# Kernel optimization log

Hardware: AMD Instinct MI355X
Metric: run time of the kernel (lower is better)

Reference implementation:

```python
import jax, jax.numpy as jnp
import numpy as np

HEADS = 4
KS = 7          # neighborhood kernel size
EPS = 1e-5
C = 64
N, H, W = 8, 64, 64


def _gather_idx(L, k):
    # NATTEN-style neighborhood: window centered at pixel, shifted to stay in bounds.
    start = jnp.clip(jnp.arange(L) - k // 2, 0, L - k)            # [L]
    idx = start[:, None] + jnp.arange(k)                           # [L, k] absolute neighbor idx
    # relative-position-bias index: (query - neighbor) + (k-1) in [0, 2k-2]
    rel = (jnp.arange(L) - start)[:, None] + (k - 1) - jnp.arange(k)[None, :]  # [L, k]
    return idx, rel


def na2d(x, qkv_w, qkv_b, rpb, proj_w, proj_b):
    # x: [N, H, W, C] -> neighborhood attention with rel-pos bias
    n, h, w, c = x.shape
    hd = c // HEADS
    scale = hd ** -0.5
    qkv = (x @ qkv_w.T + qkv_b).reshape(n, h, w, 3, HEADS, hd)
    q = qkv[..., 0, :, :] * scale                                  # [n,h,w,heads,hd]
    k = qkv[..., 1, :, :]
    v = qkv[..., 2, :, :]
    idx_h, rel_h = _gather_idx(h, KS)
    idx_w, rel_w = _gather_idx(w, KS)
    # gather neighborhoods: [n, h, k, w, k, heads, hd]
    kg = k[:, idx_h][:, :, :, idx_w]
    vg = v[:, idx_h][:, :, :, idx_w]
    attn = jnp.einsum('nijhd,niajbhd->nijhab', q, kg)              # [n,h,w,heads,k,k]
    bias = rpb[:, rel_h, :]                                        # [heads, h, k, 2k-1]
    bias = jnp.take(bias, rel_w, axis=-1)                          # [heads, h, k, w, k]
    bias = jnp.transpose(bias, (1, 3, 0, 2, 4))                    # [h, w, heads, k, k]
    attn = attn + bias
    a = jax.nn.softmax(attn.reshape(n, h, w, HEADS, KS * KS), axis=-1).reshape(attn.shape)
    out = jnp.einsum('nijhab,niajbhd->nijhd', a, vg).reshape(n, h, w, c)
    return out @ proj_w.T + proj_b


def setup_inputs() -> dict:
    key = jax.random.key(0)
    ks = jax.random.split(key, 12)
    s = 0.02
    return {
        'x': jax.random.normal(ks[0], (N, C, H, W), jnp.float32),
        'gn_w': jnp.ones((C,), jnp.float32),
        'gn_b': jnp.zeros((C,), jnp.float32),
        'qkv_w': jax.random.normal(ks[1], (3 * C, C), jnp.float32) * s,
        'qkv_b': jnp.zeros((3 * C,), jnp.float32),
        'rpb': jax.random.normal(ks[2], (HEADS, 2 * KS - 1, 2 * KS - 1), jnp.float32) * s,
        'proj_w': jax.random.normal(ks[3], (C, C), jnp.float32) * s,
        'proj_b': jnp.zeros((C,), jnp.float32),
        'ln_w': jnp.ones((C,), jnp.float32),
        'ln_b': jnp.zeros((C,), jnp.float32),
        'fc1_w': jax.random.normal(ks[4], (4 * C, C), jnp.float32) * s,
        'fc1_b': jnp.zeros((4 * C,), jnp.float32),
        'fc2_w': jax.random.normal(ks[5], (C, 4 * C), jnp.float32) * s,
        'fc2_b': jnp.zeros((C,), jnp.float32),
    }


def reference(x, gn_w, gn_b, qkv_w, qkv_b, rpb, proj_w, proj_b,
              ln_w, ln_b, fc1_w, fc1_b, fc2_w, fc2_b):
    n, c, h, w = x.shape
    x1 = jnp.transpose(x, (0, 2, 3, 1))                            # residual, NHWC
    # GroupNorm(1, C): normalize over (C,H,W) per sample, per-channel affine
    mu = jnp.mean(x, axis=(1, 2, 3), keepdims=True)
    var = jnp.var(x, axis=(1, 2, 3), keepdims=True)
    xg = (x - mu) * jax.lax.rsqrt(var + EPS)
    xg = xg * gn_w[None, :, None, None] + gn_b[None, :, None, None]
    xg = jnp.transpose(xg, (0, 2, 3, 1))                           # NHWC
    y = na2d(xg, qkv_w, qkv_b, rpb, proj_w, proj_b) + x1           # [n,h,w,c]
    y = y.reshape(n, h * w, c)
    # LayerNorm over channels + MLP (GELU), residual
    mu2 = jnp.mean(y, axis=-1, keepdims=True)
    var2 = jnp.var(y, axis=-1, keepdims=True)
    yn = (y - mu2) * jax.lax.rsqrt(var2 + EPS) * ln_w + ln_b
    hdn = jax.nn.gelu(yn @ fc1_w.T + fc1_b, approximate=False)
    y = y + (hdn @ fc2_w.T + fc2_b)
    return jnp.transpose(y.reshape(n, h, w, c), (0, 3, 1, 2))      # back to NCHW
```

## Files before the change

kernel.cpp:

```cpp
#include <hip/hip_runtime.h>
#include <math.h>

#define NSAMP 8
#define CH 64
#define HH 64
#define WW 64
#define SPATIAL 4096
#define PER_SAMPLE 262144
#define NTOK 32768
#define NHEADS 4
#define HD 16
#define KS 7
#define EPS 1e-5f
#define QSCALE 0.25f

typedef __attribute__((ext_vector_type(8))) short short8;
typedef __attribute__((ext_vector_type(4))) float f32x4;
typedef _Float16 hf2 __attribute__((ext_vector_type(2)));

__device__ __forceinline__ unsigned short f2bf(float f) {
    unsigned u = __float_as_uint(f);
    u = u + 0x7fffu + ((u >> 16) & 1u);
    return (unsigned short)(u >> 16);
}
__device__ __forceinline__ unsigned pack2(float a, float b) {
    return (unsigned)f2bf(a) | ((unsigned)f2bf(b) << 16);
}
__device__ __forceinline__ unsigned short f2h(float f) {
    _Float16 h = (_Float16)f;
    return __builtin_bit_cast(unsigned short, h);
}
__device__ __forceinline__ unsigned pack2h(float a, float b) {
    return (unsigned)f2h(a) | ((unsigned)f2h(b) << 16);
}
__device__ __forceinline__ hf2 u2h(unsigned u) { return __builtin_bit_cast(hf2, u); }

__device__ __forceinline__ float dot8_h(uint4 k, uint4 q) {
    hf2 a0 = u2h(k.x), a1 = u2h(k.y), a2 = u2h(k.z), a3 = u2h(k.w);
    hf2 b0 = u2h(q.x), b1 = u2h(q.y), b2 = u2h(q.z), b3 = u2h(q.w);
    float s;
    s = (float)a0.x * (float)b0.x;
    s = fmaf((float)a0.y, (float)b0.y, s);
    s = fmaf((float)a1.x, (float)b1.x, s);
    s = fmaf((float)a1.y, (float)b1.y, s);
    s = fmaf((float)a2.x, (float)b2.x, s);
    s = fmaf((float)a2.y, (float)b2.y, s);
    s = fmaf((float)a3.x, (float)b3.x, s);
    s = fmaf((float)a3.y, (float)b3.y, s);
    return s;
}
__device__ __forceinline__ void pv8_h(uint4 v, float p, float* acc) {
    hf2 a0 = u2h(v.x), a1 = u2h(v.y), a2 = u2h(v.z), a3 = u2h(v.w);
    acc[0] = fmaf(p, (float)a0.x, acc[0]);
    acc[1] = fmaf(p, (float)a0.y, acc[1]);
    acc[2] = fmaf(p, (float)a1.x, acc[2]);
    acc[3] = fmaf(p, (float)a1.y, acc[3]);
    acc[4] = fmaf(p, (float)a2.x, acc[4]);
    acc[5] = fmaf(p, (float)a2.y, acc[5]);
    acc[6] = fmaf(p, (float)a3.x, acc[6]);
    acc[7] = fmaf(p, (float)a3.y, acc[7]);
}

__global__ __launch_bounds__(256) void k_statsprep(const float* __restrict__ x,
                                                   float* __restrict__ stats,
                                                   const float* __restrict__ qkv_w,
                                                   const float* __restrict__ fc1_w,
                                                   const float* __restrict__ fc2_w,
                                                   const float* __restrict__ proj_w,
                                                   unsigned short* __restrict__ wb) {
    int blk = blockIdx.x;
    if (blk >= 256) {
        int i = (blk - 256) * 256 + threadIdx.x;
        if (i < 12288)      wb[i] = f2bf(qkv_w[i]);
        else if (i < 28672) wb[i] = f2bf(fc1_w[i - 12288]);
        else if (i < 45056) wb[i] = f2bf(fc2_w[i - 28672]);
        else                wb[i] = f2bf(proj_w[i - 45056]);
        return;
    }
    int n = blk >> 5, chunk = blk & 31;
    const float4* p4 = (const float4*)(x + n * PER_SAMPLE + chunk * 8192);
    int t = threadIdx.x;
    float s1 = 0.f, s2 = 0.f;
#pragma unroll
    for (int i = 0; i < 8; i++) {
        float4 v = p4[t + i * 256];
        s1 += v.x + v.y + v.z + v.w;
        s2 += v.x * v.x + v.y * v.y + v.z * v.z + v.w * v.w;
    }
#pragma unroll
    for (int off = 1; off < 64; off <<= 1) {
        s1 += __shfl_xor(s1, off);
        s2 += __shfl_xor(s2, off);
    }
    __shared__ float r1[4], r2[4];
    int lane = t & 63, wv = t >> 6;
    if (lane == 0) { r1[wv] = s1; r2[wv] = s2; }
    __syncthreads();
    if (t == 0) {
        stats[(n * 32 + chunk) * 2 + 0] = r1[0] + r1[1] + r1[2] + r1[3];
        stats[(n * 32 + chunk) * 2 + 1] = r2[0] + r2[1] + r2[2] + r2[3];
    }
}

__global__ __launch_bounds__(256) void k_qkv(const float* __restrict__ x,
                                             const float* __restrict__ stats,
                                             const float* __restrict__ gn_w,
                                             const float* __restrict__ gn_b,
                                             const unsigned short* __restrict__ qkv_wb,
                                             const float* __restrict__ qkv_b,
                                             uint4* __restrict__ qb8,
                                             uint4* __restrict__ kvb8) {
    __shared__ __attribute__((aligned(16))) short xA[4 * 2 * 64 * 8];
    __shared__ float obuf[4][16 * 65];
    int s0 = blockIdx.x * 64;
    int smp = s0 >> 12, sp = s0 & 4095;
    int t = threadIdx.x, tok = t & 63, g = t >> 6;

    float ps1 = 0.f, ps2 = 0.f;
    {
        const float2* pp = (const float2*)stats + smp * 32;
#pragma unroll
        for (int i = 0; i < 32; i++) {
            float2 p = pp[i];
            ps1 += p.x;
            ps2 += p.y;
        }
    }
    float mu = ps1 * (1.f / (float)PER_SAMPLE);
    float var = ps2 * (1.f / (float)PER_SAMPLE) - mu * mu;
    float rstd = rsqrtf(var + EPS);

    {
        const float* xp = x + smp * PER_SAMPLE + sp + tok;
        float v[16];
#pragma unroll
        for (int i = 0; i < 16; i++) {
            int c = g * 16 + i;
            v[i] = (xp[(size_t)c * SPATIAL] - mu) * rstd * gn_w[c] + gn_b[c];
        }
#pragma unroll
        for (int e = 0; e < 2; e++) {
            int cb = 2 * g + e;
            int kf = cb >> 2, qq = cb & 3;
            uint4 p;
            p.x = pack2(v[e * 8 + 0], v[e * 8 + 1]);
            p.y = pack2(v[e * 8 + 2], v[e * 8 + 3]);
            p.z = pack2(v[e * 8 + 4], v[e * 8 + 5]);
            p.w = pack2(v[e * 8 + 6], v[e * 8 + 7]);
            int chunk = ((tok >> 4) * 2 + kf) * 64 + (tok & 15) + (qq << 4);
            *(uint4*)&xA[chunk * 8] = p;
        }
    }
    __syncthreads();

    int w = __builtin_amdgcn_readfirstlane(g);
    int lane = t & 63, nh = lane & 15, qd = lane >> 4;

    short8 af[8];
#pragma unroll
    for (int mt = 0; mt < 4; mt++)
#pragma unroll
        for (int kf = 0; kf < 2; kf++)
            af[mt * 2 + kf] = *(const short8*)&xA[((mt * 2 + kf) * 64 + lane) * 8];

    for (int nt = 0; nt < 3; nt++) {
        int n0 = w * 48 + nt * 16;
        const unsigned short* wp = qkv_wb + (size_t)(n0 + nh) * 64 + qd * 8;
        short8 b0 = *(const short8*)(wp);
        short8 b1 = *(const short8*)(wp + 32);
        float bias = qkv_b[n0 + nh];
        bool isq = (n0 < 64);
        f32x4 acc[4];
#pragma unroll
        for (int mt = 0; mt < 4; mt++) {
            f32x4 d = {0.f, 0.f, 0.f, 0.f};
            d = __builtin_amdgcn_mfma_f32_16x16x32_bf16(af[mt * 2 + 0], b0, d, 0, 0, 0);
            d = __builtin_amdgcn_mfma_f32_16x16x32_bf16(af[mt * 2 + 1], b1, d, 0, 0, 0);
            acc[mt] = d;
        }
#pragma unroll
        for (int mt = 0; mt < 4; mt++)
#pragma unroll
            for (int r = 0; r < 4; r++) {
                float vv = acc[mt][r] + bias;
                if (isq) vv *= QSCALE;
                obuf[w][nh * 65 + mt * 16 + qd * 4 + r] = vv;
            }
        __builtin_amdgcn_wave_barrier();
#pragma unroll
        for (int u = 0; u < 2; u++) {
            uint4 p;
            p.x = pack2h(obuf[w][(u * 8 + 0) * 65 + lane], obuf[w][(u * 8 + 1) * 65 + lane]);
            p.y = pack2h(obuf[w][(u * 8 + 2) * 65 + lane], obuf[w][(u * 8 + 3) * 65 + lane]);
            p.z = pack2h(obuf[w][(u * 8 + 4) * 65 + lane], obuf[w][(u * 8 + 5) * 65 + lane]);
            p.w = pack2h(obuf[w][(u * 8 + 6) * 65 + lane], obuf[w][(u * 8 + 7) * 65 + lane]);
            if (n0 < 64)
                qb8[(size_t)((n0 >> 3) + u) * NTOK + s0 + lane] = p;
            else if (n0 < 128)
                kvb8[(size_t)(((n0 - 64) >> 3) + u) * NTOK + s0 + lane] = p;
            else
                kvb8[(size_t)(8 + ((n0 - 128) >> 3) + u) * NTOK + s0 + lane] = p;
        }
        __builtin_amdgcn_wave_barrier();
    }
}

__global__ __launch_bounds__(256, 4) void k_fused(const uint4* __restrict__ qb8,
                                               const uint4* __restrict__ kvb8,
                                               const float* __restrict__ rpb,
                                               const unsigned short* __restrict__ proj_wb,
                                               const float* __restrict__ proj_b,
                                               const float* __restrict__ x,
                                               const float* __restrict__ ln_w,
                                               const float* __restrict__ ln_b,
                                               const unsigned short* __restrict__ fc1_wb,
                                               const float* __restrict__ fc1_b,
                                               const unsigned short* __restrict__ fc2_wb,
                                               const float* __restrict__ fc2_b,
                                               float* __restrict__ out) {
    __shared__ __attribute__((aligned(16))) short fragA[2 * 2 * 64 * 8];
    __shared__ __attribute__((aligned(16))) short lhA[2 * 8 * 64 * 8];
    __shared__ float obuf[4][16 * 33];
    __shared__ float red1[256], red2[256];
    int xcd = blockIdx.x & 7, idx = blockIdx.x >> 3;
    int half = idx & 1;
    int h = xcd * 8 + ((idx >> 1) & 7);
    int n = idx >> 4;
    int t = threadIdx.x, lane = t & 63;
    int g = __builtin_amdgcn_readfirstlane(t >> 6);
    int w2 = lane & 31;
    int dh = lane >> 5;
    int w = half * 32 + w2;
    int rowbase = n * 4096 + h * 64;
    int cb = 2 * g + dh;

    uint4 qa = qb8[(size_t)cb * NTOK + rowbase + w];
    int sh = min(max(h - 3, 0), HH - KS);
    int sw = min(max(w - 3, 0), WW - KS);

    float sum = 0.f;
    float acc[8];
#pragma unroll
    for (int i = 0; i < 8; i++) acc[i] = 0.f;

#pragma unroll
    for (int a = 0; a < 7; a++) {
        int nb = n * 4096 + (sh + a) * 64 + sw;
        const float* rp = rpb + (g * 13 + (h - sh + 6 - a)) * 13 + (w - sw + 6);
        const uint4* kp = kvb8 + (size_t)cb * NTOK + nb;
        const uint4* vp = kvb8 + (size_t)(8 + cb) * NTOK + nb;
#pragma unroll
        for (int bb = 0; bb < 7; bb++) {
            uint4 kv = kp[bb];
            uint4 vv = vp[bb];
            float dhalf = dot8_h(kv, qa);
            float d = dhalf + __shfl_xor(dhalf, 32);
            d += rp[-bb];
            float e = __expf(d);
            sum += e;
            pv8_h(vv, e, acc);
        }
    }
    float rs = 1.f / sum;

    const float* xr = x + n * PER_SAMPLE + h * 64 + w;
    float xres[8];
#pragma unroll
    for (int i = 0; i < 8; i++)
        xres[i] = xr[(size_t)(cb * 8 + i) * SPATIAL];

    {
        int kf = cb >> 2, qsel = cb & 3;
        uint4 p;
        p.x = pack2(acc[0] * rs, acc[1] * rs);
        p.y = pack2(acc[2] * rs, acc[3] * rs);
        p.z = pack2(acc[4] * rs, acc[5] * rs);
        p.w = pack2(acc[6] * rs, acc[7] * rs);
        *(uint4*)&fragA[(((w2 >> 4) * 2 + kf) * 64 + (w2 & 15) + (qsel << 4)) * 8] = p;
    }
    __syncthreads();

    int nh = lane & 15, qd = lane >> 4;
    float yreg[8];
    {
        short8 af[4];
#pragma unroll
        for (int mt = 0; mt < 2; mt++)
#pragma unroll
            for (int kf = 0; kf < 2; kf++)
                af[mt * 2 + kf] = *(const short8*)&fragA[((mt * 2 + kf) * 64 + lane) * 8];

        int n0 = g * 16;
        const unsigned short* wp = proj_wb + (size_t)(n0 + nh) * 64 + qd * 8;
        short8 b0 = *(const short8*)(wp);
        short8 b1 = *(const short8*)(wp + 32);
        float bias = proj_b[n0 + nh];
#pragma unroll
        for (int mt = 0; mt < 2; mt++) {
            f32x4 d = {0.f, 0.f, 0.f, 0.f};
            d = __builtin_amdgcn_mfma_f32_16x16x32_bf16(af[mt * 2 + 0], b0, d, 0, 0, 0);
            d = __builtin_amdgcn_mfma_f32_16x16x32_bf16(af[mt * 2 + 1], b1, d, 0, 0, 0);
#pragma unroll
            for (int r = 0; r < 4; r++)
                obuf[g][nh * 33 + mt * 16 + qd * 4 + r] = d[r] + bias;
        }
        __builtin_amdgcn_wave_barrier();
#pragma unroll
        for (int i = 0; i < 8; i++)
            yreg[i] = obuf[g][(dh * 8 + i) * 33 + w2] + xres[i];
    }

    {
        float s1 = 0.f, s2 = 0.f;
#pragma unroll
        for (int i = 0; i < 8; i++) { s1 += yreg[i]; s2 += yreg[i] * yreg[i]; }
        red1[t] = s1;
        red2[t] = s2;
        __syncthreads();
        float m1 = 0.f, m2 = 0.f;
#pragma unroll
        for (int u = 0; u < 8; u++) { m1 += red1[u * 32 + w2]; m2 += red2[u * 32 + w2]; }
        float mu = m1 * (1.f / 64.f);
        float rstd = rsqrtf(m2 * (1.f / 64.f) - mu * mu + EPS);
        float v[8];
#pragma unroll
        for (int i = 0; i < 8; i++) {
            int c = cb * 8 + i;
            v[i] = (yreg[i] - mu) * rstd * ln_w[c] + ln_b[c];
        }
        int kf = cb >> 2, qsel = cb & 3;
        uint4 p;
        p.x = pack2(v[0], v[1]);
        p.y = pack2(v[2], v[3]);
        p.z = pack2(v[4], v[5]);
        p.w = pack2(v[6], v[7]);
        *(uint4*)&fragA[(((w2 >> 4) * 2 + kf) * 64 + (w2 & 15) + (qsel << 4)) * 8] = p;
    }
    __syncthreads();

    {
        short8 yf[4];
#pragma unroll
        for (int mt = 0; mt < 2; mt++)
#pragma unroll
            for (int kf = 0; kf < 2; kf++)
                yf[mt * 2 + kf] = *(const short8*)&fragA[((mt * 2 + kf) * 64 + lane) * 8];

#pragma unroll
        for (int nt = 0; nt < 4; nt++) {
            int n0f = g * 64 + nt * 16;
            const unsigned short* wp = fc1_wb + (size_t)(n0f + nh) * 64 + qd * 8;
            short8 b0 = *(const short8*)(wp);
            short8 b1 = *(const short8*)(wp + 32);
            float bias = fc1_b[n0f + nh];
            int j = n0f + nh;
            int kfA = j >> 5, q2 = (j >> 3) & 3, jb = j & 7;
#pragma unroll
            for (int mt = 0; mt < 2; mt++) {
                f32x4 d = {0.f, 0.f, 0.f, 0.f};
                d = __builtin_amdgcn_mfma_f32_16x16x32_bf16(yf[mt * 2 + 0], b0, d, 0, 0, 0);
                d = __builtin_amdgcn_mfma_f32_16x16x32_bf16(yf[mt * 2 + 1], b1, d, 0, 0, 0);
#pragma unroll
                for (int r = 0; r < 4; r++) {
                    float hv = d[r] + bias;
                    float t2 = -1.5957691216f * fmaf(0.044715f * hv * hv, hv, hv);
                    hv = hv / (1.f + __expf(t2));
                    lhA[((mt * 8 + kfA) * 64 + (qd * 4 + r) + (q2 << 4)) * 8 + jb] = (short)f2bf(hv);
                }
            }
        }
    }
    __syncthreads();

    f32x4 acc2[2];
    acc2[0] = (f32x4){0.f, 0.f, 0.f, 0.f};
    acc2[1] = (f32x4){0.f, 0.f, 0.f, 0.f};
#pragma unroll
    for (int kfA = 0; kfA < 8; kfA++) {
        const unsigned short* wp = fc2_wb + (size_t)(g * 16 + nh) * 256 + kfA * 32 + qd * 8;
        short8 bb = *(const short8*)(wp);
#pragma unroll
        for (int mt = 0; mt < 2; mt++) {
            short8 a = *(const short8*)&lhA[((mt * 8 + kfA) * 64 + lane) * 8];
            acc2[mt] = __builtin_amdgcn_mfma_f32_16x16x32_bf16(a, bb, acc2[mt], 0, 0, 0);
        }
    }
#pragma unroll
    for (int mt = 0; mt < 2; mt++)
#pragma unroll
        for (int r = 0; r < 4; r++)
            obuf[g][nh * 33 + mt * 16 + qd * 4 + r] = acc2[mt][r];
    __builtin_amdgcn_wave_barrier();
    float* op = out + (size_t)n * PER_SAMPLE + h * 64 + w;
#pragma unroll
    for (int i = 0; i < 8; i++) {
        int c = cb * 8 + i;
        op[(size_t)c * SPATIAL] = obuf[g][(dh * 8 + i) * 33 + w2] + fc2_b[c] + yreg[i];
    }
}

extern "C" void kernel_launch(void* const* d_in, const int* in_sizes, int n_in,
                              void* d_out, int out_size, void* d_ws, size_t ws_size,
                              hipStream_t stream) {
    const float* x      = (const float*)d_in[0];
    const float* gn_w   = (const float*)d_in[1];
    const float* gn_b   = (const float*)d_in[2];
    const float* qkv_w  = (const float*)d_in[3];
    const float* qkv_b  = (const float*)d_in[4];
    const float* rpb    = (const float*)d_in[5];
    const float* proj_w = (const float*)d_in[6];
    const float* proj_b = (const float*)d_in[7];
    const float* ln_w   = (const float*)d_in[8];
    const float* ln_b   = (const float*)d_in[9];
    const float* fc1_w  = (const float*)d_in[10];
    const float* fc1_b  = (const float*)d_in[11];
    const float* fc2_w  = (const float*)d_in[12];
    const float* fc2_b  = (const float*)d_in[13];
    float* out = (float*)d_out;

    float* ws    = (float*)d_ws;
    float* stats = ws;
    uint4* qb8   = (uint4*)(ws + 512);
    uint4* kvb8  = qb8 + (size_t)8 * NTOK;
    unsigned short* wb = (unsigned short*)(kvb8 + (size_t)16 * NTOK);
    unsigned short* qkv_wb  = wb;
    unsigned short* fc1_wb  = wb + 12288;
    unsigned short* fc2_wb  = wb + 28672;
    unsigned short* proj_wb = wb + 45056;

    k_statsprep<<<448, 256, 0, stream>>>(x, stats, qkv_w, fc1_w, fc2_w, proj_w, wb);
    k_qkv      <<<512, 256, 0, stream>>>(x, stats, gn_w, gn_b, qkv_wb, qkv_b, qb8, kvb8);
    k_fused    <<<1024, 256, 0, stream>>>(qb8, kvb8, rpb, proj_wb, proj_b, x,
                                          ln_w, ln_b, fc1_wb, fc1_b, fc2_wb, fc2_b, out);
}
```

Baseline: 123.1 us.

## Split fused attention+MLP kernel across 512 threads with 4-dim per-lane work

Doubles the fused kernel's block size to 512 threads. Each lane now handles 4 head dims instead of 8, with an extra cross-lane shuffle to complete the dot product. The MFMA stages are split so each wave pair processes one 16-token tile instead of two. The aim is more parallelism and latency hiding in the neighborhood attention loop. The cost is extra shuffles, narrower 8-byte loads, and more LDS for the reduction buffers.

```diff
diff --git a/kernel.cpp b/kernel.cpp
--- a/kernel.cpp
+++ b/kernel.cpp
@@ -35,30 +35,22 @@
 }
 __device__ __forceinline__ hf2 u2h(unsigned u) { return __builtin_bit_cast(hf2, u); }
 
-__device__ __forceinline__ float dot8_h(uint4 k, uint4 q) {
-    hf2 a0 = u2h(k.x), a1 = u2h(k.y), a2 = u2h(k.z), a3 = u2h(k.w);
-    hf2 b0 = u2h(q.x), b1 = u2h(q.y), b2 = u2h(q.z), b3 = u2h(q.w);
+__device__ __forceinline__ float dot4_h(uint2 k, uint2 q) {
+    hf2 a0 = u2h(k.x), a1 = u2h(k.y);
+    hf2 b0 = u2h(q.x), b1 = u2h(q.y);
     float s;
     s = (float)a0.x * (float)b0.x;
     s = fmaf((float)a0.y, (float)b0.y, s);
     s = fmaf((float)a1.x, (float)b1.x, s);
     s = fmaf((float)a1.y, (float)b1.y, s);
-    s = fmaf((float)a2.x, (float)b2.x, s);
-    s = fmaf((float)a2.y, (float)b2.y, s);
-    s = fmaf((float)a3.x, (float)b3.x, s);
-    s = fmaf((float)a3.y, (float)b3.y, s);
     return s;
 }
-__device__ __forceinline__ void pv8_h(uint4 v, float p, float* acc) {
-    hf2 a0 = u2h(v.x), a1 = u2h(v.y), a2 = u2h(v.z), a3 = u2h(v.w);
+__device__ __forceinline__ void pv4_h(uint2 v, float p, float* acc) {
+    hf2 a0 = u2h(v.x), a1 = u2h(v.y);
     acc[0] = fmaf(p, (float)a0.x, acc[0]);
     acc[1] = fmaf(p, (float)a0.y, acc[1]);
     acc[2] = fmaf(p, (float)a1.x, acc[2]);
     acc[3] = fmaf(p, (float)a1.y, acc[3]);
-    acc[4] = fmaf(p, (float)a2.x, acc[4]);
-    acc[5] = fmaf(p, (float)a2.y, acc[5]);
-    acc[6] = fmaf(p, (float)a3.x, acc[6]);
-    acc[7] = fmaf(p, (float)a3.y, acc[7]);
 }
 
 __global__ __launch_bounds__(256) void k_statsprep(const float* __restrict__ x,
@@ -205,7 +197,7 @@
     }
 }
 
-__global__ __launch_bounds__(256, 4) void k_fused(const uint4* __restrict__ qb8,
+__global__ __launch_bounds__(512, 8) void k_fused(const uint4* __restrict__ qb8,
                                                const uint4* __restrict__ kvb8,
                                                const float* __restrict__ rpb,
                                                const unsigned short* __restrict__ proj_wb,
@@ -220,132 +212,126 @@
                                                float* __restrict__ out) {
     __shared__ __attribute__((aligned(16))) short fragA[2 * 2 * 64 * 8];
     __shared__ __attribute__((aligned(16))) short lhA[2 * 8 * 64 * 8];
-    __shared__ float obuf[4][16 * 33];
-    __shared__ float red1[256], red2[256];
+    __shared__ float obuf[8][16 * 17];
+    __shared__ float red1[512], red2[512];
     int xcd = blockIdx.x & 7, idx = blockIdx.x >> 3;
     int half = idx & 1;
     int h = xcd * 8 + ((idx >> 1) & 7);
     int n = idx >> 4;
     int t = threadIdx.x, lane = t & 63;
-    int g = __builtin_amdgcn_readfirstlane(t >> 6);
-    int w2 = lane & 31;
-    int dh = lane >> 5;
+    int g2 = __builtin_amdgcn_readfirstlane(t >> 6);
+    int g = g2 >> 1;
+    int th = g2 & 1;
+    int w2t = lane & 15;
+    int q = lane >> 4;
+    int w2 = th * 16 + w2t;
     int w = half * 32 + w2;
     int rowbase = n * 4096 + h * 64;
-    int cb = 2 * g + dh;
-
-    uint4 qa = qb8[(size_t)cb * NTOK + rowbase + w];
+    int cb = 2 * g + (q >> 1);
+    int qsub = q & 1;
+
+    uint2 qa = ((const uint2*)qb8)[((size_t)cb * NTOK + rowbase + w) * 2 + qsub];
     int sh = min(max(h - 3, 0), HH - KS);
     int sw = min(max(w - 3, 0), WW - KS);
+    const uint2* kp2 = (const uint2*)(kvb8 + (size_t)cb * NTOK);
+    const uint2* vp2 = (const uint2*)(kvb8 + (size_t)(8 + cb) * NTOK);
 
     float sum = 0.f;
-    float acc[8];
-#pragma unroll
-    for (int i = 0; i < 8; i++) acc[i] = 0.f;
+    float acc[4];
+#pragma unroll
+    for (int i = 0; i < 4; i++) acc[i] = 0.f;
 
 #pragma unroll
     for (int a = 0; a < 7; a++) {
         int nb = n * 4096 + (sh + a) * 64 + sw;
         const float* rp = rpb + (g * 13 + (h - sh + 6 - a)) * 13 + (w - sw + 6);
-        const uint4* kp = kvb8 + (size_t)cb * NTOK + nb;
-        const uint4* vp = kvb8 + (size_t)(8 + cb) * NTOK + nb;
 #pragma unroll
         for (int bb = 0; bb < 7; bb++) {
-            uint4 kv = kp[bb];
-            uint4 vv = vp[bb];
-            float dhalf = dot8_h(kv, qa);
-            float d = dhalf + __shfl_xor(dhalf, 32);
+            uint2 kv = kp2[(size_t)(nb + bb) * 2 + qsub];
+            uint2 vv = vp2[(size_t)(nb + bb) * 2 + qsub];
+            float dq = dot4_h(kv, qa);
+            float d = dq + __shfl_xor(dq, 16);
+            d += __shfl_xor(d, 32);
             d += rp[-bb];
             float e = __expf(d);
             sum += e;
-            pv8_h(vv, e, acc);
+            pv4_h(vv, e, acc);
         }
     }
     float rs = 1.f / sum;
 
     const float* xr = x + n * PER_SAMPLE + h * 64 + w;
-    float xres[8];
-#pragma unroll
-    for (int i = 0; i < 8; i++)
-        xres[i] = xr[(size_t)(cb * 8 + i) * SPATIAL];
-
-    {
-        int kf = cb >> 2, qsel = cb & 3;
-        uint4 p;
-        p.x = pack2(acc[0] * rs, acc[1] * rs);
-        p.y = pack2(acc[2] * rs, acc[3] * rs);
-        p.z = pack2(acc[4] * rs, acc[5] * rs);
-        p.w = pack2(acc[6] * rs, acc[7] * rs);
-        *(uint4*)&fragA[(((w2 >> 4) * 2 + kf) * 64 + (w2 & 15) + (qsel << 4)) * 8] = p;
+    float xres[4];
+#pragma unroll
+    for (int i = 0; i < 4; i++)
+        xres[i] = xr[(size_t)(g * 16 + q * 4 + i) * SPATIAL];
+
+    int kf = cb >> 2, qsel = cb & 3;
+    int chunk = ((w2 >> 4) * 2 + kf) * 64 + (w2 & 15) + (qsel << 4);
+    {
+        uint2 p2;
+        p2.x = pack2(acc[0] * rs, acc[1] * rs);
+        p2.y = pack2(acc[2] * rs, acc[3] * rs);
+        *(uint2*)&fragA[chunk * 8 + qsub * 4] = p2;
     }
     __syncthreads();
 
     int nh = lane & 15, qd = lane >> 4;
-    float yreg[8];
-    {
-        short8 af[4];
-#pragma unroll
-        for (int mt = 0; mt < 2; mt++)
-#pragma unroll
-            for (int kf = 0; kf < 2; kf++)
-                af[mt * 2 + kf] = *(const short8*)&fragA[((mt * 2 + kf) * 64 + lane) * 8];
-
+    float yreg[4];
+    {
+        short8 af0 = *(const short8*)&fragA[((th * 2 + 0) * 64 + lane) * 8];
+        short8 af1 = *(const short8*)&fragA[((th * 2 + 1) * 64 + lane) * 8];
         int n0 = g * 16;
         const unsigned short* wp = proj_wb + (size_t)(n0 + nh) * 64 + qd * 8;
         short8 b0 = *(const short8*)(wp);
         short8 b1 = *(const short8*)(wp + 32);
         float bias = proj_b[n0 + nh];
-#pragma unroll
-        for (int mt = 0; mt < 2; mt++) {
-            f32x4 d = {0.f, 0.f, 0.f, 0.f};
-            d = __builtin_amdgcn_mfma_f32_16x16x32_bf16(af[mt * 2 + 0], b0, d, 0, 0, 0);
-            d = __builtin_amdgcn_mfma_f32_16x16x32_bf16(af[mt * 2 + 1], b1, d, 0, 0, 0);
-#pragma unroll
-            for (int r = 0; r < 4; r++)
-                obuf[g][nh * 33 + mt * 16 + qd * 4 + r] = d[r] + bias;
-        }
+        f32x4 d = {0.f, 0.f, 0.f, 0.f};
+        d = __builtin_amdgcn_mfma_f32_16x16x32_bf16(af0, b0, d, 0, 0, 0);
+        d = __builtin_amdgcn_mfma_f32_16x16x32_bf16(af1, b1, d, 0, 0, 0);
+#pragma unroll
+        for (int r = 0; r < 4; r++)
+            obuf[g2][nh * 17 + qd * 4 + r] = d[r] + bias;
         __builtin_amdgcn_wave_barrier();
 #pragma unroll
-        for (int i = 0; i < 8; i++)
-            yreg[i] = obuf[g][(dh * 8 + i) * 33 + w2] + xres[i];
+        for (int i = 0; i < 4; i++)
+            yreg[i] = obuf[g2][(q * 4 + i) * 17 + w2t] + xres[i];
     }
 
     {
         float s1 = 0.f, s2 = 0.f;
 #pragma unroll
-        for (int i = 0; i < 8; i++) { s1 += yreg[i]; s2 += yreg[i] * yreg[i]; }
+        for (int i = 0; i < 4; i++) { s1 += yreg[i]; s2 += yreg[i] * yreg[i]; }
         red1[t] = s1;
         red2[t] = s2;
         __syncthreads();
         float m1 = 0.f, m2 = 0.f;
 #pragma unroll
-        for (int u = 0; u < 8; u++) { m1 += red1[u * 32 + w2]; m2 += red2[u * 32 + w2]; }
+        for (int gg = 0; gg < 4; gg++)
+#pragma unroll
+            for (int qq = 0; qq < 4; qq++) {
+                int tt = (gg * 2 + th) * 64 + qq * 16 + w2t;
+                m1 += red1[tt];
+                m2 += red2[tt];
+            }
         float mu = m1 * (1.f / 64.f);
         float rstd = rsqrtf(m2 * (1.f / 64.f) - mu * mu + EPS);
-        float v[8];
-#pragma unroll
-        for (int i = 0; i < 8; i++) {
-            int c = cb * 8 + i;
+        float v[4];
+#pragma unroll
+        for (int i = 0; i < 4; i++) {
+            int c = g * 16 + q * 4 + i;
             v[i] = (yreg[i] - mu) * rstd * ln_w[c] + ln_b[c];
         }
-        int kf = cb >> 2, qsel = cb & 3;
-        uint4 p;
-        p.x = pack2(v[0], v[1]);
-        p.y = pack2(v[2], v[3]);
-        p.z = pack2(v[4], v[5]);
-        p.w = pack2(v[6], v[7]);
-        *(uint4*)&fragA[(((w2 >> 4) * 2 + kf) * 64 + (w2 & 15) + (qsel << 4)) * 8] = p;
+        uint2 p2;
+        p2.x = pack2(v[0], v[1]);
+        p2.y = pack2(v[2], v[3]);
+        *(uint2*)&fragA[chunk * 8 + qsub * 4] = p2;
     }
     __syncthreads();
 
     {
-        short8 yf[4];
-#pragma unroll
-        for (int mt = 0; mt < 2; mt++)
-#pragma unroll
-            for (int kf = 0; kf < 2; kf++)
-                yf[mt * 2 + kf] = *(const short8*)&fragA[((mt * 2 + kf) * 64 + lane) * 8];
-
+        short8 yf0 = *(const short8*)&fragA[((th * 2 + 0) * 64 + lane) * 8];
+        short8 yf1 = *(const short8*)&fragA[((th * 2 + 1) * 64 + lane) * 8];
 #pragma unroll
         for (int nt = 0; nt < 4; nt++) {
             int n0f = g * 64 + nt * 16;
@@ -354,48 +340,38 @@
             short8 b1 = *(const short8*)(wp + 32);
             float bias = fc1_b[n0f + nh];
             int j = n0f + nh;
-            int kfA = j >> 5, q2 = (j >> 3) & 3, jb = j & 7;
-#pragma unroll
-            for (int mt = 0; mt < 2; mt++) {
-                f32x4 d = {0.f, 0.f, 0.f, 0.f};
-                d = __builtin_amdgcn_mfma_f32_16x16x32_bf16(yf[mt * 2 + 0], b0, d, 0, 0, 0);
-                d = __builtin_amdgcn_mfma_f32_16x16x32_bf16(yf[mt * 2 + 1], b1, d, 0, 0, 0);
-#pragma unroll
-                for (int r = 0; r < 4; r++) {
-                    float hv = d[r] + bias;
-                    float t2 = -1.5957691216f * fmaf(0.044715f * hv * hv, hv, hv);
-                    hv = hv / (1.f + __expf(t2));
-                    lhA[((mt * 8 + kfA) * 64 + (qd * 4 + r) + (q2 << 4)) * 8 + jb] = (short)f2bf(hv);
-                }
+            int kfA = j >> 5, q2j = (j >> 3) & 3, jb = j & 7;
+            f32x4 d = {0.f, 0.f, 0.f, 0.f};
+            d = __builtin_amdgcn_mfma_f32_16x16x32_bf16(yf0, b0, d, 0, 0, 0);
+            d = __builtin_amdgcn_mfma_f32_16x16x32_bf16(yf1, b1, d, 0, 0, 0);
+#pragma unroll
+            for (int r = 0; r < 4; r++) {
+                float hv = d[r] + bias;
+                float t2 = -1.5957691216f * fmaf(0.044715f * hv * hv, hv, hv);
+                hv = hv / (1.f + __expf(t2));
+                lhA[((th * 8 + kfA) * 64 + (qd * 4 + r) + (q2j << 4)) * 8 + jb] = (short)f2bf(hv);
             }
         }
     }
     __syncthreads();
 
-    f32x4 acc2[2];
-    acc2[0] = (f32x4){0.f, 0.f, 0.f, 0.f};
-    acc2[1] = (f32x4){0.f, 0.f, 0.f, 0.f};
+    f32x4 acc2 = {0.f, 0.f, 0.f, 0.f};
 #pragma unroll
     for (int kfA = 0; kfA < 8; kfA++) {
         const unsigned short* wp = fc2_wb + (size_t)(g * 16 + nh) * 256 + kfA * 32 + qd * 8;
-        short8 bb = *(const short8*)(wp);
-#pragma unroll
-        for (int mt = 0; mt < 2; mt++) {
-            short8 a = *(const short8*)&lhA[((mt * 8 + kfA) * 64 + lane) * 8];
-            acc2[mt] = __builtin_amdgcn_mfma_f32_16x16x32_bf16(a, bb, acc2[mt], 0, 0, 0);
-        }
-    }
-#pragma unroll
-    for (int mt = 0; mt < 2; mt++)
-#pragma unroll
-        for (int r = 0; r < 4; r++)
-            obuf[g][nh * 33 + mt * 16 + qd * 4 + r] = acc2[mt][r];
+        short8 bw = *(const short8*)(wp);
+        short8 a = *(const short8*)&lhA[((th * 8 + kfA) * 64 + lane) * 8];
+        acc2 = __builtin_amdgcn_mfma_f32_16x16x32_bf16(a, bw, acc2, 0, 0, 0);
+    }
+#pragma unroll
+    for (int r = 0; r < 4; r++)
+        obuf[g2][nh * 17 + qd * 4 + r] = acc2[r];
     __builtin_amdgcn_wave_barrier();
     float* op = out + (size_t)n * PER_SAMPLE + h * 64 + w;
 #pragma unroll
-    for (int i = 0; i < 8; i++) {
-        int c = cb * 8 + i;
-        op[(size_t)c * SPATIAL] = obuf[g][(dh * 8 + i) * 33 + w2] + fc2_b[c] + yreg[i];
+    for (int i = 0; i < 4; i++) {
+        int c = g * 16 + q * 4 + i;
+        op[(size_t)c * SPATIAL] = obuf[g2][(q * 4 + i) * 17 + w2t] + fc2_b[c] + yreg[i];
     }
 }
 
@@ -430,6 +406,6 @@
 
     k_statsprep<<<448, 256, 0, stream>>>(x, stats, qkv_w, fc1_w, fc2_w, proj_w, wb);
     k_qkv      <<<512, 256, 0, stream>>>(x, stats, gn_w, gn_b, qkv_wb, qkv_b, qb8, kvb8);
-    k_fused    <<<1024, 256, 0, stream>>>(qb8, kvb8, rpb, proj_wb, proj_b, x,
+    k_fused    <<<1024, 512, 0, stream>>>(qb8, kvb8, rpb, proj_wb, proj_b, x,
                                           ln_w, ln_b, fc1_wb, fc1_b, fc2_wb, fc2_b, out);
 }
```

Measured after the change: 166.9 us. 1.36x slower.
